# Performance work log

Hardware: AMD Instinct MI355X
Metric: run time of the kernel (lower is better)

Reference implementation:

```python
import jax, jax.numpy as jnp
import numpy as np

B, T, F, H, O = 1024, 512, 64, 32, 1


def setup_inputs() -> dict:
    key = jax.random.key(0)
    ks = jax.random.split(key, 8)
    s = lambda *sh: 1.0 / np.sqrt(sh[0])
    return {
        "x": jax.random.normal(ks[0], (B, T, F), jnp.float32),
        "W_enc": jax.random.normal(ks[1], (F, F), jnp.float32) * s(F),
        "b_enc": jnp.zeros((F,), jnp.float32),
        "kernel": jax.random.normal(ks[2], (F, 4 * H), jnp.float32) * s(F),
        "recurrent": jax.random.normal(ks[3], (H, 4 * H), jnp.float32) * s(H),
        "bias": jnp.zeros((4 * H,), jnp.float32),
        "attn_W": jax.random.normal(ks[4], (H, H), jnp.float32) * s(H),
        "attn_b": jnp.zeros((H,), jnp.float32),
        "attn_u": jax.random.normal(ks[5], (H,), jnp.float32) * s(H),
        "W_dec": jax.random.normal(ks[6], (2 * H, O), jnp.float32) * s(2 * H),
        "b_dec": jnp.zeros((O,), jnp.float32),
    }


def _lstm(enc, kernel, recurrent, bias):
    # enc: [B,T,F] -> rnn_out [B,T,H]; Keras gate order i,f,c,o
    H_ = recurrent.shape[0]
    xg = jnp.einsum('btf,fg->tbg', enc, kernel) + bias  # precompute input gates, time-major

    def step(carry, xg_t):
        h, c = carry
        z = xg_t + h @ recurrent  # [B,4H]
        i, f, g, o = jnp.split(z, 4, axis=-1)
        i, f, o = jax.nn.sigmoid(i), jax.nn.sigmoid(f), jax.nn.sigmoid(o)
        c = f * c + i * jnp.tanh(g)
        h = o * jnp.tanh(c)
        return (h, c), h

    Bv = enc.shape[0]
    init = (jnp.zeros((Bv, H_), enc.dtype), jnp.zeros((Bv, H_), enc.dtype))
    _, hs = jax.lax.scan(step, init, xg)
    return jnp.transpose(hs, (1, 0, 2))  # [B,T,H]


def reference(x, W_enc, b_enc, kernel, recurrent, bias, attn_W, attn_b, attn_u, W_dec, b_dec):
    enc = jnp.tanh(x @ W_enc + b_enc)                       # [B,T,F]
    rnn_out = _lstm(enc, kernel, recurrent, bias)           # [B,T,H]
    latent = jnp.tanh(rnn_out @ attn_W + attn_b)            # [B,T,H]
    score = jax.nn.softmax(latent @ attn_u, axis=-1)        # [B,T]
    pooled = jnp.einsum('bth,bt->bh', rnn_out, score)       # [B,H]
    out = jnp.concatenate([rnn_out[:, -1, :], pooled], axis=1)  # [B,2H]
    return jax.nn.sigmoid(out @ W_dec + b_dec)              # [B,O]
```

## Files before the change

### kernel.cpp

```cpp
#include <hip/hip_runtime.h>
#include <stdint.h>

#define B_ 1024
#define T_ 512
#define F_ 64
#define H_ 32
#define G_ 128

typedef __attribute__((ext_vector_type(8))) short bf16x8;
typedef __attribute__((ext_vector_type(4))) float f32x4;

__device__ __forceinline__ uint32_t bf16r(float f) {
  uint32_t u = __builtin_bit_cast(uint32_t, f);
  return (u + 0x7fffu + ((u >> 16) & 1u)) >> 16;
}
__device__ __forceinline__ float rl(float v, int l) {
  return __builtin_bit_cast(float, __builtin_amdgcn_readlane(__builtin_bit_cast(int, v), l));
}
__device__ __forceinline__ float fsig(float x) { return 1.f / (1.f + __expf(-x)); }
__device__ __forceinline__ float ftanh(float x) { return 2.f / (1.f + __expf(-2.f * x)) - 1.f; }
__device__ __forceinline__ float bflo(uint32_t d) { return __builtin_bit_cast(float, d << 16); }
__device__ __forceinline__ float bfhi(uint32_t d) { return __builtin_bit_cast(float, d & 0xffff0000u); }

#define MFMA16(a, b, c) __builtin_amdgcn_mfma_f32_16x16x32_bf16((a), (b), (c), 0, 0, 0)

__global__ __launch_bounds__(256, 3) void k1_mfma(
    const float* __restrict__ x, const float* __restrict__ Wenc,
    const float* __restrict__ benc, const float* __restrict__ kern,
    const float* __restrict__ bias, uint32_t* __restrict__ xg) {
  __shared__ unsigned short sWt[64 * 72];
  __shared__ unsigned short sKt[128 * 72];
  __shared__ unsigned short sE[128 * 72];
  const int tid = threadIdx.x;
  const int lane = tid & 63;
  const int w = tid >> 6;
  const int m = lane & 15;
  const int g = lane >> 4;
  const int r0 = blockIdx.x * 128;

  {
    const int r = tid & 63;
    const int c0 = (tid >> 6) * 16;
#pragma unroll
    for (int q = 0; q < 4; ++q) {
      float4 v = *(const float4*)(Wenc + (size_t)r * F_ + c0 + q * 4);
      sWt[(c0 + q * 4 + 0) * 72 + r] = (unsigned short)bf16r(v.x);
      sWt[(c0 + q * 4 + 1) * 72 + r] = (unsigned short)bf16r(v.y);
      sWt[(c0 + q * 4 + 2) * 72 + r] = (unsigned short)bf16r(v.z);
      sWt[(c0 + q * 4 + 3) * 72 + r] = (unsigned short)bf16r(v.w);
    }
    const int d0 = (tid >> 6) * 32;
#pragma unroll
    for (int q = 0; q < 8; ++q) {
      float4 v = *(const float4*)(kern + (size_t)r * G_ + d0 + q * 4);
      sKt[(d0 + q * 4 + 0) * 72 + r] = (unsigned short)bf16r(v.x);
      sKt[(d0 + q * 4 + 1) * 72 + r] = (unsigned short)bf16r(v.y);
      sKt[(d0 + q * 4 + 2) * 72 + r] = (unsigned short)bf16r(v.z);
      sKt[(d0 + q * 4 + 3) * 72 + r] = (unsigned short)bf16r(v.w);
    }
  }
  __syncthreads();

  bf16x8 a[2][2];
#pragma unroll
  for (int rt = 0; rt < 2; ++rt)
#pragma unroll
    for (int kh = 0; kh < 2; ++kh) {
      const float* xr = x + (size_t)(r0 + w * 32 + rt * 16 + m) * F_ + kh * 32 + g * 8;
      float4 v0 = ((const float4*)xr)[0];
      float4 v1 = ((const float4*)xr)[1];
      bf16x8 t;
      t[0] = (short)bf16r(v0.x); t[1] = (short)bf16r(v0.y);
      t[2] = (short)bf16r(v0.z); t[3] = (short)bf16r(v0.w);
      t[4] = (short)bf16r(v1.x); t[5] = (short)bf16r(v1.y);
      t[6] = (short)bf16r(v1.z); t[7] = (short)bf16r(v1.w);
      a[rt][kh] = t;
    }

#pragma unroll
  for (int ct = 0; ct < 4; ++ct) {
    float be = benc[ct * 16 + m];
    f32x4 acc0 = {be, be, be, be};
    f32x4 acc1 = {be, be, be, be};
    bf16x8 b0 = *(const bf16x8*)&sWt[(ct * 16 + m) * 72 + g * 8];
    bf16x8 b1 = *(const bf16x8*)&sWt[(ct * 16 + m) * 72 + 32 + g * 8];
    acc0 = MFMA16(a[0][0], b0, acc0);
    acc0 = MFMA16(a[0][1], b1, acc0);
    acc1 = MFMA16(a[1][0], b0, acc1);
    acc1 = MFMA16(a[1][1], b1, acc1);
#pragma unroll
    for (int r4 = 0; r4 < 4; ++r4) {
      sE[(w * 32 + g * 4 + r4) * 72 + ct * 16 + m] =
          (unsigned short)bf16r(ftanh(acc0[r4]));
      sE[(w * 32 + 16 + g * 4 + r4) * 72 + ct * 16 + m] =
          (unsigned short)bf16r(ftanh(acc1[r4]));
    }
  }
  __syncthreads();

  bf16x8 e[2][2];
#pragma unroll
  for (int rt = 0; rt < 2; ++rt)
#pragma unroll
    for (int kh = 0; kh < 2; ++kh)
      e[rt][kh] = *(const bf16x8*)&sE[(w * 32 + rt * 16 + m) * 72 + kh * 32 + g * 8];

#pragma unroll
  for (int ctp = 0; ctp < 4; ++ctp) {
    float blo = bias[ctp * 16 + m];
    float bhi = bias[64 + ctp * 16 + m];
    f32x4 lo0 = {blo, blo, blo, blo}, lo1 = {blo, blo, blo, blo};
    f32x4 hi0 = {bhi, bhi, bhi, bhi}, hi1 = {bhi, bhi, bhi, bhi};
    bf16x8 bl0 = *(const bf16x8*)&sKt[(ctp * 16 + m) * 72 + g * 8];
    bf16x8 bl1 = *(const bf16x8*)&sKt[(ctp * 16 + m) * 72 + 32 + g * 8];
    bf16x8 bh0 = *(const bf16x8*)&sKt[(64 + ctp * 16 + m) * 72 + g * 8];
    bf16x8 bh1 = *(const bf16x8*)&sKt[(64 + ctp * 16 + m) * 72 + 32 + g * 8];
    lo0 = MFMA16(e[0][0], bl0, lo0);  lo0 = MFMA16(e[0][1], bl1, lo0);
    lo1 = MFMA16(e[1][0], bl0, lo1);  lo1 = MFMA16(e[1][1], bl1, lo1);
    hi0 = MFMA16(e[0][0], bh0, hi0);  hi0 = MFMA16(e[0][1], bh1, hi0);
    hi1 = MFMA16(e[1][0], bh0, hi1);  hi1 = MFMA16(e[1][1], bh1, hi1);
#pragma unroll
    for (int r4 = 0; r4 < 4; ++r4) {
      int row0 = r0 + w * 32 + g * 4 + r4;
      xg[(size_t)row0 * 64 + ctp * 16 + m] =
          bf16r(lo0[r4]) | (bf16r(hi0[r4]) << 16);
      int row1 = row0 + 16;
      xg[(size_t)row1 * 64 + ctp * 16 + m] =
          bf16r(lo1[r4]) | (bf16r(hi1[r4]) << 16);
    }
  }
}

__global__ __launch_bounds__(64, 1) void k2_scan(
    const uint32_t* __restrict__ xgin, float* __restrict__ hout,
    const float* __restrict__ rec) {
  const int lane = threadIdx.x;
  const int b = blockIdx.x;
  const bool lo32 = (lane < 32);

  float rA[H_], rB[H_];
#pragma unroll
  for (int k = 0; k < H_; ++k) {
    rA[k] = rec[k * G_ + lane];
    rB[k] = rec[k * G_ + 64 + lane];
  }

  const uint32_t* xp = xgin + (size_t)b * (T_ * 64) + lane;
  float* hst = hout + (size_t)b * (T_ * 64);

  float h = 0.f, c = 0.f;

  auto step = [&](uint32_t w, int t) {
    float z1a = bflo(w);
    float z2a = bfhi(w);
    float z1b = 0.f, z1c = 0.f, z1d = 0.f;
    float z2b = 0.f, z2c = 0.f, z2d = 0.f;
#pragma unroll
    for (int k4 = 0; k4 < 8; ++k4) {
      float s0 = rl(h, 4 * k4 + 0);
      float s1 = rl(h, 4 * k4 + 1);
      float s2 = rl(h, 4 * k4 + 2);
      float s3 = rl(h, 4 * k4 + 3);
      z1a += s0 * rA[4 * k4 + 0];  z2a += s0 * rB[4 * k4 + 0];
      z1b += s1 * rA[4 * k4 + 1];  z2b += s1 * rB[4 * k4 + 1];
      z1c += s2 * rA[4 * k4 + 2];  z2c += s2 * rB[4 * k4 + 2];
      z1d += s3 * rA[4 * k4 + 3];  z2d += s3 * rB[4 * k4 + 3];
    }
    float z1 = (z1a + z1b) + (z1c + z1d);
    float z2 = (z2a + z2b) + (z2c + z2d);

    float act1 = fsig(z1);
    float xx = lo32 ? 2.f * z2 : z2;
    float sg = fsig(xx);
    float act2 = lo32 ? 2.f * sg - 1.f : sg;

    float f_all = __shfl(act1, lane | 32);
    float o_all = __shfl(act2, lane | 32);

    c = f_all * c + act1 * act2;
    float tc = ftanh(c);
    h = o_all * tc;

    if (lo32) hst[(size_t)t * 64 + lane] = h;
  };

  uint32_t p[8];
#pragma unroll
  for (int i = 0; i < 8; ++i) p[i] = xp[i * 64];
  for (int tb = 0; tb < T_; tb += 8) {
    uint32_t n[8];
#pragma unroll
    for (int i = 0; i < 8; ++i) n[i] = xp[((tb + 8 + i) & 511) * 64];
#pragma unroll
    for (int i = 0; i < 8; ++i) step(p[i], tb + i);
#pragma unroll
    for (int i = 0; i < 8; ++i) p[i] = n[i];
  }
}

__global__ __launch_bounds__(256, 4) void k3_attn(
    const uint32_t* __restrict__ xg,
    const float* __restrict__ attnW, const float* __restrict__ attnB,
    const float* __restrict__ attnU, const float* __restrict__ Wdec,
    const float* __restrict__ bdec, float* __restrict__ out) {
  __shared__ float sSc[T_];
  __shared__ float sRed[8];
  __shared__ float sP[8][H_];
  const int tid = threadIdx.x;
  const int b = blockIdx.x;

  const uint32_t* hbase = xg + (size_t)b * (T_ * 64);

  float mysc[2];
#pragma unroll
  for (int q = 0; q < 2; ++q) {
    int t = tid + q * 256;
    const float4* hp = (const float4*)(hbase + (size_t)t * 64);

    float hv[H_];
#pragma unroll
    for (int i = 0; i < 8; ++i) {
      float4 v = hp[i];
      hv[4 * i + 0] = v.x; hv[4 * i + 1] = v.y;
      hv[4 * i + 2] = v.z; hv[4 * i + 3] = v.w;
    }

    float lat[H_];
#pragma unroll
    for (int j4 = 0; j4 < 8; ++j4) {
      float4 bv = ((const float4*)attnB)[j4];
      lat[4 * j4 + 0] = bv.x; lat[4 * j4 + 1] = bv.y;
      lat[4 * j4 + 2] = bv.z; lat[4 * j4 + 3] = bv.w;
    }
#pragma unroll
    for (int d = 0; d < H_; ++d) {
      float hd = hv[d];
      const float4* wr = (const float4*)(attnW + d * H_);
#pragma unroll
      for (int j4 = 0; j4 < 8; ++j4) {
        float4 w = wr[j4];
        lat[4 * j4 + 0] += hd * w.x;
        lat[4 * j4 + 1] += hd * w.y;
        lat[4 * j4 + 2] += hd * w.z;
        lat[4 * j4 + 3] += hd * w.w;
      }
    }
    float sc = 0.f;
#pragma unroll
    for (int j = 0; j < H_; ++j) sc += ftanh(lat[j]) * attnU[j];
    mysc[q] = sc;
  }

  float m2 = fmaxf(mysc[0], mysc[1]);
  m2 = fmaxf(m2, __shfl_xor(m2, 1));  m2 = fmaxf(m2, __shfl_xor(m2, 2));
  m2 = fmaxf(m2, __shfl_xor(m2, 4));  m2 = fmaxf(m2, __shfl_xor(m2, 8));
  m2 = fmaxf(m2, __shfl_xor(m2, 16)); m2 = fmaxf(m2, __shfl_xor(m2, 32));
  if ((tid & 63) == 0) sRed[tid >> 6] = m2;
  __syncthreads();
  float m = fmaxf(fmaxf(sRed[0], sRed[1]), fmaxf(sRed[2], sRed[3]));
  float e0 = __expf(mysc[0] - m), e1 = __expf(mysc[1] - m);
  sSc[tid] = e0;
  sSc[tid + 256] = e1;
  float s2 = e0 + e1;
  s2 += __shfl_xor(s2, 1);  s2 += __shfl_xor(s2, 2);
  s2 += __shfl_xor(s2, 4);  s2 += __shfl_xor(s2, 8);
  s2 += __shfl_xor(s2, 16); s2 += __shfl_xor(s2, 32);
  if ((tid & 63) == 0) sRed[4 + (tid >> 6)] = s2;
  __syncthreads();
  float l = (sRed[4] + sRed[5]) + (sRed[6] + sRed[7]);

  const int j = tid & 31;
  const int grp = tid >> 5;
  float p = 0.f;
  for (int tt = grp * 64; tt < grp * 64 + 64; ++tt) {
    p += sSc[tt] * ((const float*)(hbase + (size_t)tt * 64))[j];
  }
  sP[grp][j] = p;
  __syncthreads();

  if (tid < H_) {
    float pooled = 0.f;
#pragma unroll
    for (int g = 0; g < 8; ++g) pooled += sP[g][tid];
    pooled /= l;
    float h511 = ((const float*)(hbase + (size_t)511 * 64))[tid];
    float val = h511 * Wdec[tid] + pooled * Wdec[H_ + tid];
    val += __shfl_xor(val, 1);  val += __shfl_xor(val, 2);
    val += __shfl_xor(val, 4);  val += __shfl_xor(val, 8);
    val += __shfl_xor(val, 16);
    if (tid == 0) out[b] = fsig(val + bdec[0]);
  }
}

extern "C" void kernel_launch(void* const* d_in, const int* in_sizes, int n_in,
                              void* d_out, int out_size, void* d_ws, size_t ws_size,
                              hipStream_t stream) {
  const float* x     = (const float*)d_in[0];
  const float* Wenc  = (const float*)d_in[1];
  const float* benc  = (const float*)d_in[2];
  const float* kern  = (const float*)d_in[3];
  const float* rec   = (const float*)d_in[4];
  const float* bias  = (const float*)d_in[5];
  const float* attnW = (const float*)d_in[6];
  const float* attnB = (const float*)d_in[7];
  const float* attnU = (const float*)d_in[8];
  const float* Wdec  = (const float*)d_in[9];
  const float* bdec  = (const float*)d_in[10];

  uint32_t* xg = (uint32_t*)d_ws;

  hipLaunchKernelGGL(k1_mfma, dim3((B_ * T_) / 128), dim3(256), 0, stream,
                     x, Wenc, benc, kern, bias, xg);
  hipLaunchKernelGGL(k2_scan, dim3(B_), dim3(64), 0, stream,
                     xg, (float*)d_ws, rec);
  hipLaunchKernelGGL(k3_attn, dim3(B_), dim3(256), 0, stream,
                     xg, attnW, attnB, attnU, Wdec, bdec, (float*)d_out);
}
```

Before: 421.0 us.

## Batch 16 sequences per wave in LSTM scan using bf16 MFMA recurrence

The recurrent scan kernel now handles 16 batch rows per 64-lane wave. The h·recurrent product runs as eight 16x16x32 bf16 MFMAs per timestep, replacing 32 readlane broadcasts and scalar FMAs per lane. The new hidden state is repacked to bf16 and redistributed with shuffles to form the next MFMA B fragment, and all four gates are evaluated per lane. This removes the per-step readlane/FMA chain, but the grid drops to 64 waves, leaving most CUs idle. The recurrent weights and h are also rounded to bf16, which lowers precision inside the recurrence.

```diff
diff --git a/kernel.cpp b/kernel.cpp
--- a/kernel.cpp
+++ b/kernel.cpp
@@ -9,13 +9,11 @@
 
 typedef __attribute__((ext_vector_type(8))) short bf16x8;
 typedef __attribute__((ext_vector_type(4))) float f32x4;
+typedef __attribute__((ext_vector_type(4))) unsigned int u32x4;
 
 __device__ __forceinline__ uint32_t bf16r(float f) {
   uint32_t u = __builtin_bit_cast(uint32_t, f);
   return (u + 0x7fffu + ((u >> 16) & 1u)) >> 16;
-}
-__device__ __forceinline__ float rl(float v, int l) {
-  return __builtin_bit_cast(float, __builtin_amdgcn_readlane(__builtin_bit_cast(int, v), l));
 }
 __device__ __forceinline__ float fsig(float x) { return 1.f / (1.f + __expf(-x)); }
 __device__ __forceinline__ float ftanh(float x) { return 2.f / (1.f + __expf(-2.f * x)) - 1.f; }
@@ -131,71 +129,103 @@
   }
 }
 
-__global__ __launch_bounds__(64, 1) void k2_scan(
-    const uint32_t* __restrict__ xgin, float* __restrict__ hout,
-    const float* __restrict__ rec) {
+__global__ __attribute__((amdgpu_flat_work_group_size(64, 64)))
+__attribute__((amdgpu_waves_per_eu(1, 1)))
+void k2_scan(const uint32_t* __restrict__ xgin, float* __restrict__ hout,
+             const float* __restrict__ rec) {
   const int lane = threadIdx.x;
-  const int b = blockIdx.x;
-  const bool lo32 = (lane < 32);
-
-  float rA[H_], rB[H_];
-#pragma unroll
-  for (int k = 0; k < H_; ++k) {
-    rA[k] = rec[k * G_ + lane];
-    rB[k] = rec[k * G_ + 64 + lane];
-  }
-
-  const uint32_t* xp = xgin + (size_t)b * (T_ * 64) + lane;
-  float* hst = hout + (size_t)b * (T_ * 64);
-
-  float h = 0.f, c = 0.f;
-
-  auto step = [&](uint32_t w, int t) {
-    float z1a = bflo(w);
-    float z2a = bfhi(w);
-    float z1b = 0.f, z1c = 0.f, z1d = 0.f;
-    float z2b = 0.f, z2c = 0.f, z2d = 0.f;
-#pragma unroll
-    for (int k4 = 0; k4 < 8; ++k4) {
-      float s0 = rl(h, 4 * k4 + 0);
-      float s1 = rl(h, 4 * k4 + 1);
-      float s2 = rl(h, 4 * k4 + 2);
-      float s3 = rl(h, 4 * k4 + 3);
-      z1a += s0 * rA[4 * k4 + 0];  z2a += s0 * rB[4 * k4 + 0];
-      z1b += s1 * rA[4 * k4 + 1];  z2b += s1 * rB[4 * k4 + 1];
-      z1c += s2 * rA[4 * k4 + 2];  z2c += s2 * rB[4 * k4 + 2];
-      z1d += s3 * rA[4 * k4 + 3];  z2d += s3 * rB[4 * k4 + 3];
-    }
-    float z1 = (z1a + z1b) + (z1c + z1d);
-    float z2 = (z2a + z2b) + (z2c + z2d);
-
-    float act1 = fsig(z1);
-    float xx = lo32 ? 2.f * z2 : z2;
-    float sg = fsig(xx);
-    float act2 = lo32 ? 2.f * sg - 1.f : sg;
-
-    float f_all = __shfl(act1, lane | 32);
-    float o_all = __shfl(act2, lane | 32);
-
-    c = f_all * c + act1 * act2;
-    float tc = ftanh(c);
-    h = o_all * tc;
-
-    if (lo32) hst[(size_t)t * 64 + lane] = h;
+  const int m = lane & 15;
+  const int g = lane >> 4;
+  const int b0 = blockIdx.x * 16;
+
+  bf16x8 a[8];
+#pragma unroll
+  for (int n = 0; n < 8; ++n) {
+    bf16x8 t;
+#pragma unroll
+    for (int j = 0; j < 8; ++j)
+      t[j] = (short)bf16r(rec[(size_t)(8 * g + j) * G_ + n * 16 + m]);
+    a[n] = t;
+  }
+
+  const uint32_t* xp = xgin + (size_t)(b0 + m) * (T_ * 64) + g * 4;
+  float* hp = hout + (size_t)(b0 + m) * (T_ * 64) + g * 4;
+
+  const int lane02 = m + ((g & 1) ? 32 : 0);
+  const int lane13 = lane02 + 16;
+  const bool glo = (g < 2);
+
+  f32x4 c_lo = {0.f, 0.f, 0.f, 0.f}, c_hi = {0.f, 0.f, 0.f, 0.f};
+  uint32_t q0 = 0, q1 = 0, q2 = 0, q3 = 0;
+
+  auto step = [&](uint4 w0, uint4 w1, uint4 w2, uint4 w3, int t) {
+    u32x4 qq = {q0, q1, q2, q3};
+    bf16x8 bfrag = __builtin_bit_cast(bf16x8, qq);
+
+    f32x4 z0 = {bflo(w0.x), bflo(w0.y), bflo(w0.z), bflo(w0.w)};
+    f32x4 z1 = {bflo(w1.x), bflo(w1.y), bflo(w1.z), bflo(w1.w)};
+    f32x4 z2 = {bflo(w2.x), bflo(w2.y), bflo(w2.z), bflo(w2.w)};
+    f32x4 z3 = {bflo(w3.x), bflo(w3.y), bflo(w3.z), bflo(w3.w)};
+    f32x4 z4 = {bfhi(w0.x), bfhi(w0.y), bfhi(w0.z), bfhi(w0.w)};
+    f32x4 z5 = {bfhi(w1.x), bfhi(w1.y), bfhi(w1.z), bfhi(w1.w)};
+    f32x4 z6 = {bfhi(w2.x), bfhi(w2.y), bfhi(w2.z), bfhi(w2.w)};
+    f32x4 z7 = {bfhi(w3.x), bfhi(w3.y), bfhi(w3.z), bfhi(w3.w)};
+
+    z0 = MFMA16(a[0], bfrag, z0);
+    z1 = MFMA16(a[1], bfrag, z1);
+    z2 = MFMA16(a[2], bfrag, z2);
+    z3 = MFMA16(a[3], bfrag, z3);
+    z4 = MFMA16(a[4], bfrag, z4);
+    z5 = MFMA16(a[5], bfrag, z5);
+    z6 = MFMA16(a[6], bfrag, z6);
+    z7 = MFMA16(a[7], bfrag, z7);
+
+    f32x4 h_lo, h_hi;
+#pragma unroll
+    for (int r = 0; r < 4; ++r) {
+      float i1 = fsig(z0[r]), i2 = fsig(z1[r]);
+      float f1 = fsig(z2[r]), f2 = fsig(z3[r]);
+      float g1 = ftanh(z4[r]), g2 = ftanh(z5[r]);
+      float o1 = fsig(z6[r]), o2 = fsig(z7[r]);
+      c_lo[r] = f1 * c_lo[r] + i1 * g1;
+      c_hi[r] = f2 * c_hi[r] + i2 * g2;
+      h_lo[r] = o1 * ftanh(c_lo[r]);
+      h_hi[r] = o2 * ftanh(c_hi[r]);
+    }
+
+    *(float4*)(hp + (size_t)t * 64) = (float4){h_lo[0], h_lo[1], h_lo[2], h_lo[3]};
+    *(float4*)(hp + (size_t)t * 64 + 16) = (float4){h_hi[0], h_hi[1], h_hi[2], h_hi[3]};
+
+    uint32_t pr0 = bf16r(h_lo[0]) | (bf16r(h_lo[1]) << 16);
+    uint32_t pr1 = bf16r(h_lo[2]) | (bf16r(h_lo[3]) << 16);
+    uint32_t pr2 = bf16r(h_hi[0]) | (bf16r(h_hi[1]) << 16);
+    uint32_t pr3 = bf16r(h_hi[2]) | (bf16r(h_hi[3]) << 16);
+
+    uint32_t x0 = __shfl(pr0, lane02), x1 = __shfl(pr1, lane02);
+    uint32_t x2 = __shfl(pr0, lane13), x3 = __shfl(pr1, lane13);
+    uint32_t y0 = __shfl(pr2, lane02), y1 = __shfl(pr3, lane02);
+    uint32_t y2 = __shfl(pr2, lane13), y3 = __shfl(pr3, lane13);
+    q0 = glo ? x0 : y0;  q1 = glo ? x1 : y1;
+    q2 = glo ? x2 : y2;  q3 = glo ? x3 : y3;
   };
 
-  uint32_t p[8];
-#pragma unroll
-  for (int i = 0; i < 8; ++i) p[i] = xp[i * 64];
-  for (int tb = 0; tb < T_; tb += 8) {
-    uint32_t n[8];
-#pragma unroll
-    for (int i = 0; i < 8; ++i) n[i] = xp[((tb + 8 + i) & 511) * 64];
-#pragma unroll
-    for (int i = 0; i < 8; ++i) step(p[i], tb + i);
-#pragma unroll
-    for (int i = 0; i < 8; ++i) p[i] = n[i];
-  }
+#define LD4(p, tt, d0, d1, d2, d3)                                   \
+  uint4 d0 = *(const uint4*)((p) + (size_t)((tt) & 511) * 64);       \
+  uint4 d1 = *(const uint4*)((p) + (size_t)((tt) & 511) * 64 + 16);  \
+  uint4 d2 = *(const uint4*)((p) + (size_t)((tt) & 511) * 64 + 32);  \
+  uint4 d3 = *(const uint4*)((p) + (size_t)((tt) & 511) * 64 + 48);
+
+  LD4(xp, 0, A0, A1, A2, A3)
+  LD4(xp, 1, Bb0, Bb1, Bb2, Bb3)
+  for (int t = 0; t < T_; t += 2) {
+    LD4(xp, t + 2, nA0, nA1, nA2, nA3)
+    step(A0, A1, A2, A3, t);
+    A0 = nA0; A1 = nA1; A2 = nA2; A3 = nA3;
+    LD4(xp, t + 3, nB0, nB1, nB2, nB3)
+    step(Bb0, Bb1, Bb2, Bb3, t + 1);
+    Bb0 = nB0; Bb1 = nB1; Bb2 = nB2; Bb3 = nB3;
+  }
+#undef LD4
 }
 
 __global__ __launch_bounds__(256, 4) void k3_attn(
@@ -311,7 +341,7 @@
 
   hipLaunchKernelGGL(k1_mfma, dim3((B_ * T_) / 128), dim3(256), 0, stream,
                      x, Wenc, benc, kern, bias, xg);
-  hipLaunchKernelGGL(k2_scan, dim3(B_), dim3(64), 0, stream,
+  hipLaunchKernelGGL(k2_scan, dim3(B_ / 16), dim3(64), 0, stream,
                      xg, (float*)d_ws, rec);
   hipLaunchKernelGGL(k3_attn, dim3(B_), dim3(256), 0, stream,
                      xg, attnW, attnB, attnU, Wdec, bdec, (float*)d_out);
```

Measured after the change: 1.010 ms. 2.4x slower.

## Compute all four LSTM gates per lane with weights stashed in AGPRs

Applied to the files above, without the earlier changes.

The recurrent scan kernel used to split the gates across 64 lanes and exchange f/o through shuffles. Now each of the 32 hidden units is computed redundantly in both half-waves, with all four gates in the same lane. The 128 recurrent weights per lane live in accumulation registers and are read back with inline asm every step. This removes the cross-lane shuffles from the serial critical path, at the cost of twice the FMAs per lane, extra accvgpr reads each step, and a shallower prefetch (4 steps instead of 8).

```diff
diff --git a/kernel.cpp b/kernel.cpp
--- a/kernel.cpp
+++ b/kernel.cpp
@@ -131,70 +131,82 @@
   }
 }
 
-__global__ __launch_bounds__(64, 1) void k2_scan(
-    const uint32_t* __restrict__ xgin, float* __restrict__ hout,
-    const float* __restrict__ rec) {
+__global__ __attribute__((amdgpu_flat_work_group_size(64, 64)))
+__attribute__((amdgpu_waves_per_eu(1, 1)))
+void k2_scan(const uint32_t* __restrict__ xgin, float* __restrict__ hout,
+             const float* __restrict__ rec) {
   const int lane = threadIdx.x;
+  const int jj = lane & 31;
   const int b = blockIdx.x;
-  const bool lo32 = (lane < 32);
-
-  float rA[H_], rB[H_];
-#pragma unroll
-  for (int k = 0; k < H_; ++k) {
-    rA[k] = rec[k * G_ + lane];
-    rB[k] = rec[k * G_ + 64 + lane];
-  }
-
-  const uint32_t* xp = xgin + (size_t)b * (T_ * 64) + lane;
+
+#define DECL4(K) float wi##K, wf##K, wg##K, wo##K;
+  DECL4(0)  DECL4(1)  DECL4(2)  DECL4(3)  DECL4(4)  DECL4(5)  DECL4(6)  DECL4(7)
+  DECL4(8)  DECL4(9)  DECL4(10) DECL4(11) DECL4(12) DECL4(13) DECL4(14) DECL4(15)
+  DECL4(16) DECL4(17) DECL4(18) DECL4(19) DECL4(20) DECL4(21) DECL4(22) DECL4(23)
+  DECL4(24) DECL4(25) DECL4(26) DECL4(27) DECL4(28) DECL4(29) DECL4(30) DECL4(31)
+#undef DECL4
+
+#define STASH4(K) { \
+    float t0 = rec[K * G_ + jj]; \
+    float t1 = rec[K * G_ + 32 + jj]; \
+    float t2 = rec[K * G_ + 64 + jj]; \
+    float t3 = rec[K * G_ + 96 + jj]; \
+    asm volatile("v_accvgpr_write_b32 %0, %1" : "=a"(wi##K) : "v"(t0)); \
+    asm volatile("v_accvgpr_write_b32 %0, %1" : "=a"(wf##K) : "v"(t1)); \
+    asm volatile("v_accvgpr_write_b32 %0, %1" : "=a"(wg##K) : "v"(t2)); \
+    asm volatile("v_accvgpr_write_b32 %0, %1" : "=a"(wo##K) : "v"(t3)); }
+  STASH4(0)  STASH4(1)  STASH4(2)  STASH4(3)  STASH4(4)  STASH4(5)  STASH4(6)  STASH4(7)
+  STASH4(8)  STASH4(9)  STASH4(10) STASH4(11) STASH4(12) STASH4(13) STASH4(14) STASH4(15)
+  STASH4(16) STASH4(17) STASH4(18) STASH4(19) STASH4(20) STASH4(21) STASH4(22) STASH4(23)
+  STASH4(24) STASH4(25) STASH4(26) STASH4(27) STASH4(28) STASH4(29) STASH4(30) STASH4(31)
+#undef STASH4
+
+  const uint32_t* xp0 = xgin + (size_t)b * (T_ * 64) + jj;
+  const uint32_t* xp1 = xgin + (size_t)b * (T_ * 64) + 32 + jj;
   float* hst = hout + (size_t)b * (T_ * 64);
 
   float h = 0.f, c = 0.f;
 
-  auto step = [&](uint32_t w, int t) {
-    float z1a = bflo(w);
-    float z2a = bfhi(w);
-    float z1b = 0.f, z1c = 0.f, z1d = 0.f;
-    float z2b = 0.f, z2c = 0.f, z2d = 0.f;
-#pragma unroll
-    for (int k4 = 0; k4 < 8; ++k4) {
-      float s0 = rl(h, 4 * k4 + 0);
-      float s1 = rl(h, 4 * k4 + 1);
-      float s2 = rl(h, 4 * k4 + 2);
-      float s3 = rl(h, 4 * k4 + 3);
-      z1a += s0 * rA[4 * k4 + 0];  z2a += s0 * rB[4 * k4 + 0];
-      z1b += s1 * rA[4 * k4 + 1];  z2b += s1 * rB[4 * k4 + 1];
-      z1c += s2 * rA[4 * k4 + 2];  z2c += s2 * rB[4 * k4 + 2];
-      z1d += s3 * rA[4 * k4 + 3];  z2d += s3 * rB[4 * k4 + 3];
-    }
-    float z1 = (z1a + z1b) + (z1c + z1d);
-    float z2 = (z2a + z2b) + (z2c + z2d);
-
-    float act1 = fsig(z1);
-    float xx = lo32 ? 2.f * z2 : z2;
-    float sg = fsig(xx);
-    float act2 = lo32 ? 2.f * sg - 1.f : sg;
-
-    float f_all = __shfl(act1, lane | 32);
-    float o_all = __shfl(act2, lane | 32);
-
-    c = f_all * c + act1 * act2;
-    float tc = ftanh(c);
-    h = o_all * tc;
-
-    if (lo32) hst[(size_t)t * 64 + lane] = h;
+  auto step = [&](uint32_t w0, uint32_t w1, int t) {
+    float zi = bflo(w0), zg = bfhi(w0);
+    float zf = bflo(w1), zo = bfhi(w1);
+#define AC(K) { float s = rl(h, K); float vi, vf, vg, vo; \
+    asm volatile("v_accvgpr_read_b32 %0, %1" : "=v"(vi) : "a"(wi##K)); \
+    asm volatile("v_accvgpr_read_b32 %0, %1" : "=v"(vf) : "a"(wf##K)); \
+    asm volatile("v_accvgpr_read_b32 %0, %1" : "=v"(vg) : "a"(wg##K)); \
+    asm volatile("v_accvgpr_read_b32 %0, %1" : "=v"(vo) : "a"(wo##K)); \
+    zi = fmaf(s, vi, zi); zf = fmaf(s, vf, zf); \
+    zg = fmaf(s, vg, zg); zo = fmaf(s, vo, zo); }
+    AC(0)  AC(1)  AC(2)  AC(3)  AC(4)  AC(5)  AC(6)  AC(7)
+    AC(8)  AC(9)  AC(10) AC(11) AC(12) AC(13) AC(14) AC(15)
+    AC(16) AC(17) AC(18) AC(19) AC(20) AC(21) AC(22) AC(23)
+    AC(24) AC(25) AC(26) AC(27) AC(28) AC(29) AC(30) AC(31)
+#undef AC
+
+    float i_ = fsig(zi);
+    float f_ = fsig(zf);
+    float g_ = ftanh(zg);
+    float o_ = fsig(zo);
+    c = f_ * c + i_ * g_;
+    h = o_ * ftanh(c);
+
+    if (lane < 32) hst[(size_t)t * 64 + lane] = h;
   };
 
-  uint32_t p[8];
-#pragma unroll
-  for (int i = 0; i < 8; ++i) p[i] = xp[i * 64];
-  for (int tb = 0; tb < T_; tb += 8) {
-    uint32_t n[8];
-#pragma unroll
-    for (int i = 0; i < 8; ++i) n[i] = xp[((tb + 8 + i) & 511) * 64];
-#pragma unroll
-    for (int i = 0; i < 8; ++i) step(p[i], tb + i);
-#pragma unroll
-    for (int i = 0; i < 8; ++i) p[i] = n[i];
+  uint32_t p0[4], p1[4];
+#pragma unroll
+  for (int i = 0; i < 4; ++i) { p0[i] = xp0[i * 64]; p1[i] = xp1[i * 64]; }
+  for (int tb = 0; tb < T_; tb += 4) {
+    uint32_t n0[4], n1[4];
+#pragma unroll
+    for (int i = 0; i < 4; ++i) {
+      n0[i] = xp0[((tb + 4 + i) & 511) * 64];
+      n1[i] = xp1[((tb + 4 + i) & 511) * 64];
+    }
+#pragma unroll
+    for (int i = 0; i < 4; ++i) step(p0[i], p1[i], tb + i);
+#pragma unroll
+    for (int i = 0; i < 4; ++i) { p0[i] = n0[i]; p1[i] = n1[i]; }
   }
 }
 
```

Result: slower. 551.6 us (+31.0%).
